# Performance work log

Hardware: AMD Instinct MI355X
Metric: run time of the kernel (lower is better)

Reference implementation:

```python
import jax, jax.numpy as jnp
from jax import lax
import numpy as np

H = 512      # hidden_size
L = 2        # num_layers
IN = 512     # input_size
LAT = 256    # latent_size
B = 256      # batch
S = 256      # seq_length


def setup_inputs() -> dict:
    key = jax.random.key(0)
    ks = jax.random.split(key, 12)
    sd = 0.05
    return {
        "latent": jax.random.normal(ks[0], (B, LAT), dtype=jnp.float32),
        "fc_w": jax.random.normal(ks[1], (H * L * 2, LAT), dtype=jnp.float32) * sd,
        "fc_b": jnp.zeros((H * L * 2,), dtype=jnp.float32),
        "map_w": jax.random.normal(ks[2], (IN, H * 2 * L), dtype=jnp.float32) * sd,
        "map_b": jnp.zeros((IN,), dtype=jnp.float32),
        "wih0": jax.random.normal(ks[3], (4 * H, IN), dtype=jnp.float32) * sd,
        "whh0": jax.random.normal(ks[4], (4 * H, H), dtype=jnp.float32) * sd,
        "bih0": jnp.zeros((4 * H,), dtype=jnp.float32),
        "bhh0": jnp.zeros((4 * H,), dtype=jnp.float32),
        "wih1": jax.random.normal(ks[5], (4 * H, H), dtype=jnp.float32) * sd,
        "whh1": jax.random.normal(ks[6], (4 * H, H), dtype=jnp.float32) * sd,
        "bih1": jnp.zeros((4 * H,), dtype=jnp.float32),
        "bhh1": jnp.zeros((4 * H,), dtype=jnp.float32),
        "seq_length": S,
    }


def _lstm_cell(x, h, c, wih, whh, bih, bhh):
    # torch.nn.LSTMCell gate ordering: i, f, g, o
    g = x @ wih.T + bih + h @ whh.T + bhh
    i, f, gg, o = jnp.split(g, 4, axis=-1)
    c2 = jax.nn.sigmoid(f) * c + jax.nn.sigmoid(i) * jnp.tanh(gg)
    h2 = jax.nn.sigmoid(o) * jnp.tanh(c2)
    return h2, c2


def reference(latent, fc_w, fc_b, map_w, map_b,
              wih0, whh0, bih0, bhh0, wih1, whh1, bih1, bhh1, seq_length):
    bsz = latent.shape[0]
    hid = wih0.shape[0] // 4
    nl = 2
    # dec_hidden = tanh(fc(latent)) -> view(num_layers, B, 2H) -> chunk into (h, c)
    dec = jnp.tanh(latent @ fc_w.T + fc_b)            # (B, 2*L*H)
    dec = dec.reshape(nl, bsz, 2 * hid)               # row-major reinterpret, as torch .view
    h0, c0 = dec[..., :hid], dec[..., hid:]           # each (L, B, H)
    wih = (wih0, wih1); whh = (whh0, whh1)
    bih = (bih0, bih1); bhh = (bhh0, bhh1)

    def step(carry, _):
        h, c = carry
        # cat((h,c), -1).view(B, -1) -- faithful raw reshape across (layer, batch)
        fc_in = jnp.concatenate([h, c], axis=-1).reshape(bsz, -1)  # (B, 2*L*H)
        out = jax.nn.sigmoid(fc_in @ map_w.T + map_b)              # (B, IN)
        x = out
        hs, cs = [], []
        for l in range(nl):
            h2, c2 = _lstm_cell(x, h[l], c[l], wih[l], whh[l], bih[l], bhh[l])
            hs.append(h2); cs.append(c2)
            x = h2
        hn = jnp.tanh(jnp.stack(hs))   # activation_rnn
        cn = jnp.tanh(jnp.stack(cs))   # activation_fc
        return (hn, cn), out

    _, outs = lax.scan(step, (h0, c0), None, length=int(seq_length))
    return outs  # (S, B, IN)
```

## Files before the change

### kernel.cpp

```cpp
#include <hip/hip_runtime.h>

#define SEQ 256

#define WL0     0u
#define WL1     2097152u
#define FCT     4194304u
#define OFF_FC  4718592u
#define OFF_XM  5767168u
#define OFF_X0  5898240u
#define OFF_ARR 6029312u

#define S_AS0 0
#define S_WS0 8704
#define S_AS1 13312
#define S_WS1 22016
#define S_RED 13312
#define S_GS  29952
#define S_TOT 32032

__device__ __forceinline__ float sigf(float x){ return 1.0f/(1.0f + __expf(-x)); }
__device__ __forceinline__ float tanhf_(float x){
  float cx = fminf(fmaxf(x, -15.f), 15.f);
  float e = __expf(2.f*cx);
  return (e-1.f)/(e+1.f);
}

__global__ __launch_bounds__(256) void tr_kernel(const float* __restrict__ src,
                                                 float* __restrict__ dst, int R, int C){
  int i = blockIdx.x*256 + threadIdx.x;
  if (i < R*C){ int r = i / C, c = i - r*C; dst[(size_t)c*R + r] = src[i]; }
}

__global__ __launch_bounds__(256) void wprep(const float* __restrict__ wih0,
                                             const float* __restrict__ whh0,
                                             const float* __restrict__ wih1,
                                             const float* __restrict__ whh1,
                                             float* __restrict__ ws){
  const unsigned idx = blockIdx.x*256u + threadIdx.x;
  const unsigned layer = idx >> 21, rem = idx & 2097151u;
  const unsigned c = rem >> 10, k = rem & 1023u;
  const unsigned j = c >> 2, g = c & 3u;
  const float* wih = layer ? wih1 : wih0;
  const float* whh = layer ? whh1 : whh0;
  const float v = (k < 512u) ? wih[(g*512u + j)*512u + k] : whh[(g*512u + j)*512u + (k - 512u)];
  ws[(layer ? WL1 : WL0) + rem] = v;
}

__global__ __launch_bounds__(256) void init2(const float* __restrict__ latent,
                                             const float* __restrict__ fc_b,
                                             float* __restrict__ ws){
  __shared__ float ls[256];
  const int b = blockIdx.x, tid = threadIdx.x;
  if (tid < 32)
    __hip_atomic_store((unsigned*)(ws + OFF_ARR) + b*32 + tid, 0u,
                       __ATOMIC_RELAXED, __HIP_MEMORY_SCOPE_AGENT);
  ls[tid] = latent[b*256 + tid];
  __syncthreads();
  const float* fT = ws + FCT;
  for (int nc = 0; nc < 8; ++nc){
    const int n = nc*256 + tid;
    float acc = fc_b[n];
    for (int k = 0; k < 256; ++k) acc += ls[k] * fT[k*2048 + n];
    const float v = tanhf_(acc);
    const unsigned f = (unsigned)b*2048u + (unsigned)n;
    const unsigned l = f >> 18, p = (f >> 10) & 255u, q = f & 1023u;
    ws[OFF_FC + (l*128u + (p>>1))*2048u + (p&1u)*1024u + q] = v;
  }
}

__device__ __forceinline__ void gsync(unsigned* arr, unsigned epoch, int tid, int blk){
  __syncthreads();
  if (tid == 0)
    __hip_atomic_store(arr + (unsigned)blk*32u, epoch,
                       __ATOMIC_RELEASE, __HIP_MEMORY_SCOPE_AGENT);
  if (tid < 64){
    unsigned m;
    do {
      const unsigned v0 = __hip_atomic_load(arr + (unsigned)(tid      )*32u, __ATOMIC_RELAXED, __HIP_MEMORY_SCOPE_AGENT);
      const unsigned v1 = __hip_atomic_load(arr + (unsigned)(tid +  64)*32u, __ATOMIC_RELAXED, __HIP_MEMORY_SCOPE_AGENT);
      const unsigned v2 = __hip_atomic_load(arr + (unsigned)(tid + 128)*32u, __ATOMIC_RELAXED, __HIP_MEMORY_SCOPE_AGENT);
      const unsigned v3 = __hip_atomic_load(arr + (unsigned)(tid + 192)*32u, __ATOMIC_RELAXED, __HIP_MEMORY_SCOPE_AGENT);
      const unsigned m01 = v0 < v1 ? v0 : v1;
      const unsigned m23 = v2 < v3 ? v2 : v3;
      m = m01 < m23 ? m01 : m23;
      if (m < epoch) __builtin_amdgcn_s_sleep(2);
    } while (!__all(m >= epoch));
  }
  __syncthreads();
  if (tid == 0) __builtin_amdgcn_fence(__ATOMIC_ACQUIRE, "agent");
  __syncthreads();
}

__device__ __forceinline__ void fma8x8(float acc[8][8], const float4 A0, const float4 A1,
                                       const float4 W0, const float4 W1){
  const float a_[8] = {A0.x,A0.y,A0.z,A0.w,A1.x,A1.y,A1.z,A1.w};
  const float w_[8] = {W0.x,W0.y,W0.z,W0.w,W1.x,W1.y,W1.z,W1.w};
  #pragma unroll
  for (int i=0;i<8;++i)
    #pragma unroll
    for (int j=0;j<8;++j) acc[i][j] = __builtin_fmaf(a_[i], w_[j], acc[i][j]);
}

__device__ __forceinline__ void map_phase(float* sm, const float* __restrict__ FCc,
    const float* __restrict__ map_w, const float* __restrict__ map_b,
    float* __restrict__ XM, float* __restrict__ outp_t, int tid, int r0, int cb)
{
  const int rg = tid & 7;
  const int kg = tid >> 3;
  const int n0 = cb * 8;
  float acc[8][8];
  #pragma unroll
  for (int i=0;i<8;++i){
    #pragma unroll
    for (int j=0;j<8;++j) acc[i][j]=0.f;
  }
  float4 va[8]; float4 vw;

  auto LOADS = [&](int ch){
    #pragma unroll
    for (int it=0; it<8; ++it){
      const int e = tid + it*256, r = e>>5, kq = e&31;
      va[it] = *(const float4*)&FCc[(unsigned)(r0+r)*2048u + (unsigned)(ch*128 + kq*4)];
    }
    { const int n = tid>>5, kq = tid&31;
      vw = *(const float4*)&map_w[(unsigned)(n0+n)*2048u + (unsigned)(ch*128 + kq*4)]; }
  };
  auto STORES = [&](int buf){
    float* A_ = sm + (buf ? S_AS1 : S_AS0);
    float* W_ = sm + (buf ? S_WS1 : S_WS0);
    #pragma unroll
    for (int it=0; it<8; ++it){
      const int e = tid + it*256, r = e>>5, kq = e&31;
      const int col = r ^ ((kq&7)<<2);
      A_[(kq*4+0)*68 + col] = va[it].x;
      A_[(kq*4+1)*68 + col] = va[it].y;
      A_[(kq*4+2)*68 + col] = va[it].z;
      A_[(kq*4+3)*68 + col] = va[it].w;
    }
    { const int n = tid>>5, kq = tid&31;
      const int col = n ^ ((kq&7)<<2);
      W_[(kq*4+0)*36 + col] = vw.x;
      W_[(kq*4+1)*36 + col] = vw.y;
      W_[(kq*4+2)*36 + col] = vw.z;
      W_[(kq*4+3)*36 + col] = vw.w; }
  };
  auto COMPUTE = [&](int buf){
    const float* A_ = sm + (buf ? S_AS1 : S_AS0);
    const float* W_ = sm + (buf ? S_WS1 : S_WS0);
    const int phi = (kg & 7) << 2;
    const int ca0 = (rg*8) ^ phi, ca1 = ca0 ^ 4;
    #pragma unroll
    for (int u=0; u<4; ++u){
      const int k = kg*4 + u;
      const float4 a0 = *(const float4*)&A_[k*68 + ca0];
      const float4 a1 = *(const float4*)&A_[k*68 + ca1];
      const float4 w0 = *(const float4*)&W_[k*36 + phi];
      const float4 w1 = *(const float4*)&W_[k*36 + (phi^4)];
      fma8x8(acc, a0, a1, w0, w1);
    }
  };

  LOADS(0); STORES(1);
  __syncthreads();
  #pragma unroll 1
  for (int ch = 0; ch < 16; ++ch){
    const int buf = (ch & 1) ^ 1;
    if (ch+1 < 16) LOADS(ch+1);
    COMPUTE(buf);
    if (ch+1 < 16) STORES(buf^1);
    __syncthreads();
  }
  float* red = sm + S_RED;
  #pragma unroll
  for (int i=0;i<8;++i){
    #pragma unroll
    for (int j=0;j<8;++j) red[tid*65 + i*8 + j] = acc[i][j];
  }
  __syncthreads();
  #pragma unroll
  for (int s=0;s<2;++s){
    const int o = tid + s*256;
    const int r = o >> 3, nl = o & 7;
    float sum = 0.f;
    #pragma unroll
    for (int kk=0;kk<32;++kk)
      sum += red[((r>>3) + 8*kk)*65 + (r&7)*8 + nl];
    const int n = n0 + nl;
    const float v = sigf(sum + map_b[n]);
    const unsigned off = (unsigned)(r0 + r)*512u + (unsigned)n;
    XM[off] = v;
    outp_t[off] = v;
  }
}

__device__ __forceinline__ void lstm_phase(float* sm, const int l,
    const float* __restrict__ WL, const float* __restrict__ xs,
    const float* __restrict__ FCc, float* __restrict__ FCn,
    float* __restrict__ X0, const float* __restrict__ bih, const float* __restrict__ bhh,
    int tid, int r0, int cb)
{
  const int rg = tid & 7;
  const int ng = (tid >> 3) & 3;
  const int kg = tid >> 5;
  const int c0 = cb * 32;
  float acc[8][8];
  #pragma unroll
  for (int i=0;i<8;++i){
    #pragma unroll
    for (int j=0;j<8;++j) acc[i][j]=0.f;
  }
  float4 va[8], vw4[4];

  auto LOADS = [&](int ch){
    if (ch < 4){
      #pragma unroll
      for (int it=0; it<8; ++it){
        const int e = tid + it*256, r = e>>5, kq = e&31;
        va[it] = *(const float4*)&xs[(unsigned)(r0+r)*512u + (unsigned)(ch*128 + kq*4)];
      }
    } else {
      #pragma unroll
      for (int it=0; it<8; ++it){
        const int e = tid + it*256, r = e>>5, kq = e&31;
        const int b = r0 + r;
        const unsigned q = (unsigned)((ch-4)*128 + kq*4);
        va[it] = *(const float4*)&FCc[(unsigned)((l<<7) + (b>>1))*2048u + (unsigned)(b&1)*1024u + q];
      }
    }
    #pragma unroll
    for (int it=0; it<4; ++it){
      const int e = tid + it*256, n = e>>5, kq = e&31;
      vw4[it] = *(const float4*)&WL[(unsigned)(c0+n)*1024u + (unsigned)(ch*128 + kq*4)];
    }
  };
  auto STORES = [&](int buf){
    float* A_ = sm + (buf ? S_AS1 : S_AS0);
    float* W_ = sm + (buf ? S_WS1 : S_WS0);
    #pragma unroll
    for (int it=0; it<8; ++it){
      const int e = tid + it*256, r = e>>5, kq = e&31;
      const int col = r ^ ((kq&7)<<2);
      A_[(kq*4+0)*68 + col] = va[it].x;
      A_[(kq*4+1)*68 + col] = va[it].y;
      A_[(kq*4+2)*68 + col] = va[it].z;
      A_[(kq*4+3)*68 + col] = va[it].w;
    }
    #pragma unroll
    for (int it=0; it<4; ++it){
      const int e = tid + it*256, n = e>>5, kq = e&31;
      const int col = n ^ ((kq&7)<<2);
      W_[(kq*4+0)*36 + col] = vw4[it].x;
      W_[(kq*4+1)*36 + col] = vw4[it].y;
      W_[(kq*4+2)*36 + col] = vw4[it].z;
      W_[(kq*4+3)*36 + col] = vw4[it].w;
    }
  };
  auto COMPUTE = [&](int buf){
    const float* A_ = sm + (buf ? S_AS1 : S_AS0);
    const float* W_ = sm + (buf ? S_WS1 : S_WS0);
    #pragma unroll
    for (int u=0; u<16; ++u){
      const int k = kg*16 + u;
      const int s = (((kg<<2) + (u>>2)) & 7) << 2;
      const int ca = (rg*8) ^ s;
      const int cw = (ng*8) ^ s;
      const float4 a0 = *(const float4*)&A_[k*68 + ca];
      const float4 a1 = *(const float4*)&A_[k*68 + (ca^4)];
      const float4 w0 = *(const float4*)&W_[k*36 + cw];
      const float4 w1 = *(const float4*)&W_[k*36 + (cw^4)];
      fma8x8(acc, a0, a1, w0, w1);
    }
  };

  LOADS(0); STORES(1);
  __syncthreads();
  #pragma unroll 1
  for (int ch = 0; ch < 8; ++ch){
    const int buf = (ch & 1) ^ 1;
    if (ch+1 < 8) LOADS(ch+1);
    COMPUTE(buf);
    if (ch+1 < 8) STORES(buf^1);
    __syncthreads();
  }

  float* red = sm + S_RED;
  float* gs  = sm + S_GS;
  #pragma unroll
  for (int i=0;i<8;++i){
    #pragma unroll
    for (int j=0;j<8;++j) red[tid*65 + i*8 + j] = acc[i][j];
  }
  __syncthreads();
  #pragma unroll
  for (int s=0;s<8;++s){
    const int o = tid + s*256;
    const int r = o >> 5, c = o & 31;
    float sum = 0.f;
    #pragma unroll
    for (int kk=0;kk<8;++kk)
      sum += red[((r>>3) + 8*(c>>3) + 32*kk)*65 + (r&7)*8 + (c&7)];
    gs[c*65 + r] = sum;
  }
  __syncthreads();
  const int r = tid & 63, j0 = tid >> 6;
  const int row = r0 + r;
  const unsigned srow = (unsigned)((l<<7) + (row>>1))*2048u + (unsigned)(row&1)*1024u;
  #pragma unroll
  for (int jj=0;jj<2;++jj){
    const int jl = j0 + jj*4;
    const int jg = cb*8 + jl;
    const float gi = gs[(jl*4+0)*65 + r] + bih[jg]       + bhh[jg];
    const float gf = gs[(jl*4+1)*65 + r] + bih[512+jg]   + bhh[512+jg];
    const float gg = gs[(jl*4+2)*65 + r] + bih[1024+jg]  + bhh[1024+jg];
    const float go = gs[(jl*4+3)*65 + r] + bih[1536+jg]  + bhh[1536+jg];
    const float cp = FCc[srow + 512u + (unsigned)jg];
    const float c2 = sigf(gf)*cp + sigf(gi)*tanhf_(gg);
    const float h2 = sigf(go)*tanhf_(c2);
    if (l == 0) X0[(unsigned)row*512u + (unsigned)jg] = h2;
    FCn[srow + (unsigned)jg]        = tanhf_(h2);
    FCn[srow + 512u + (unsigned)jg] = tanhf_(c2);
  }
}

__launch_bounds__(256, 1)
__global__ void persist(const float* __restrict__ map_w, const float* __restrict__ map_b,
                        const float* __restrict__ bih0, const float* __restrict__ bhh0,
                        const float* __restrict__ bih1, const float* __restrict__ bhh1,
                        float* __restrict__ ws, float* __restrict__ outp)
{
  __shared__ float sm[S_TOT];
  const int tid = threadIdx.x;
  const int blk = blockIdx.x;
  const int cb = ((blk & 7) << 3) | ((blk >> 3) & 7);
  const int rb = blk >> 6;
  const int r0 = rb * 64;
  float* FC = ws + OFF_FC;
  float* XM = ws + OFF_XM;
  float* X0 = ws + OFF_X0;
  unsigned* arr = (unsigned*)(ws + OFF_ARR);
  unsigned nsync = 0;

  #pragma unroll 1
  for (int t = 0; t < SEQ; ++t){
    const unsigned cur = (unsigned)(t & 1);
    const float* FCc = FC + cur*524288u;
    float* FCn = FC + (cur^1u)*524288u;

    map_phase(sm, FCc, map_w, map_b, XM, outp + (size_t)t*131072u, tid, r0, cb);
    if (t == SEQ-1) break;
    gsync(arr, ++nsync, tid, blk);
    lstm_phase(sm, 0, ws + WL0, XM, FCc, FCn, X0, bih0, bhh0, tid, r0, cb);
    gsync(arr, ++nsync, tid, blk);
    lstm_phase(sm, 1, ws + WL1, X0, FCc, FCn, X0, bih1, bhh1, tid, r0, cb);
    gsync(arr, ++nsync, tid, blk);
  }
}

extern "C" void kernel_launch(void* const* d_in, const int* in_sizes, int n_in,
                              void* d_out, int out_size, void* d_ws, size_t ws_size,
                              hipStream_t stream)
{
  (void)in_sizes; (void)n_in; (void)out_size; (void)ws_size;
  const float* latent = (const float*)d_in[0];
  const float* fc_w   = (const float*)d_in[1];
  const float* fc_b   = (const float*)d_in[2];
  const float* map_w  = (const float*)d_in[3];
  const float* map_b  = (const float*)d_in[4];
  const float* wih0   = (const float*)d_in[5];
  const float* whh0   = (const float*)d_in[6];
  const float* bih0   = (const float*)d_in[7];
  const float* bhh0   = (const float*)d_in[8];
  const float* wih1   = (const float*)d_in[9];
  const float* whh1   = (const float*)d_in[10];
  const float* bih1   = (const float*)d_in[11];
  const float* bhh1   = (const float*)d_in[12];
  float* ws = (float*)d_ws;
  float* outp = (float*)d_out;

  tr_kernel<<<2048,256,0,stream>>>(fc_w, ws + FCT, 2048, 256);
  wprep<<<16384,256,0,stream>>>(wih0, whh0, wih1, whh1, ws);
  init2<<<256,256,0,stream>>>(latent, fc_b, ws);

  void* args[8];
  args[0] = (void*)&map_w; args[1] = (void*)&map_b;
  args[2] = (void*)&bih0;  args[3] = (void*)&bhh0;
  args[4] = (void*)&bih1;  args[5] = (void*)&bhh1;
  args[6] = (void*)&ws;    args[7] = (void*)&outp;
  hipError_t e = hipLaunchCooperativeKernel((const void*)persist, dim3(256), dim3(256),
                                            args, 0, stream);
  if (e != hipSuccess){
    persist<<<dim3(256), dim3(256), 0, stream>>>(map_w, map_b, bih0, bhh0,
                                                 bih1, bhh1, ws, outp);
  }
}
```

Baseline: 38.95 ms.

## Double threads per persistent block and halve per-thread register tile

Each persistent block now runs 512 threads instead of 256, and each thread computes an 8x4 accumulator tile instead of 8x8, with the load, store and reduction index maps rewritten to match. The aim is more latency hiding per CU during the latency-bound recurrent GEMMs, plus shorter per-thread serial FMA chains. The trade-off is a wider K-split reduction through shared memory (more partials), larger LDS scratch and more threads taking part in each barrier. The grid-wide sync code must still work with the larger block, since only the first 64 threads poll.

```diff
diff --git a/kernel.cpp b/kernel.cpp
--- a/kernel.cpp
+++ b/kernel.cpp
@@ -15,8 +15,8 @@
 #define S_AS1 13312
 #define S_WS1 22016
 #define S_RED 13312
-#define S_GS  29952
-#define S_TOT 32032
+#define S_GS  30208
+#define S_TOT 32288
 
 __device__ __forceinline__ float sigf(float x){ return 1.0f/(1.0f + __expf(-x)); }
 __device__ __forceinline__ float tanhf_(float x){
@@ -91,14 +91,14 @@
   __syncthreads();
 }
 
-__device__ __forceinline__ void fma8x8(float acc[8][8], const float4 A0, const float4 A1,
-                                       const float4 W0, const float4 W1){
+__device__ __forceinline__ void fma8x4(float acc[8][4], const float4 A0, const float4 A1,
+                                       const float4 W0){
   const float a_[8] = {A0.x,A0.y,A0.z,A0.w,A1.x,A1.y,A1.z,A1.w};
-  const float w_[8] = {W0.x,W0.y,W0.z,W0.w,W1.x,W1.y,W1.z,W1.w};
+  const float w_[4] = {W0.x,W0.y,W0.z,W0.w};
   #pragma unroll
   for (int i=0;i<8;++i)
     #pragma unroll
-    for (int j=0;j<8;++j) acc[i][j] = __builtin_fmaf(a_[i], w_[j], acc[i][j]);
+    for (int j=0;j<4;++j) acc[i][j] = __builtin_fmaf(a_[i], w_[j], acc[i][j]);
 }
 
 __device__ __forceinline__ void map_phase(float* sm, const float* __restrict__ FCc,
@@ -106,38 +106,39 @@
     float* __restrict__ XM, float* __restrict__ outp_t, int tid, int r0, int cb)
 {
   const int rg = tid & 7;
-  const int kg = tid >> 3;
+  const int ng = (tid >> 3) & 1;
+  const int kg = tid >> 4;
   const int n0 = cb * 8;
-  float acc[8][8];
+  float acc[8][4];
   #pragma unroll
   for (int i=0;i<8;++i){
     #pragma unroll
-    for (int j=0;j<8;++j) acc[i][j]=0.f;
-  }
-  float4 va[8]; float4 vw;
+    for (int j=0;j<4;++j) acc[i][j]=0.f;
+  }
+  float4 va[4]; float4 vw;
 
   auto LOADS = [&](int ch){
     #pragma unroll
-    for (int it=0; it<8; ++it){
-      const int e = tid + it*256, r = e>>5, kq = e&31;
+    for (int it=0; it<4; ++it){
+      const int e = tid + it*512, r = e>>5, kq = e&31;
       va[it] = *(const float4*)&FCc[(unsigned)(r0+r)*2048u + (unsigned)(ch*128 + kq*4)];
     }
-    { const int n = tid>>5, kq = tid&31;
+    if (tid < 256){ const int n = tid>>5, kq = tid&31;
       vw = *(const float4*)&map_w[(unsigned)(n0+n)*2048u + (unsigned)(ch*128 + kq*4)]; }
   };
   auto STORES = [&](int buf){
     float* A_ = sm + (buf ? S_AS1 : S_AS0);
     float* W_ = sm + (buf ? S_WS1 : S_WS0);
     #pragma unroll
-    for (int it=0; it<8; ++it){
-      const int e = tid + it*256, r = e>>5, kq = e&31;
+    for (int it=0; it<4; ++it){
+      const int e = tid + it*512, r = e>>5, kq = e&31;
       const int col = r ^ ((kq&7)<<2);
       A_[(kq*4+0)*68 + col] = va[it].x;
       A_[(kq*4+1)*68 + col] = va[it].y;
       A_[(kq*4+2)*68 + col] = va[it].z;
       A_[(kq*4+3)*68 + col] = va[it].w;
     }
-    { const int n = tid>>5, kq = tid&31;
+    if (tid < 256){ const int n = tid>>5, kq = tid&31;
       const int col = n ^ ((kq&7)<<2);
       W_[(kq*4+0)*36 + col] = vw.x;
       W_[(kq*4+1)*36 + col] = vw.y;
@@ -149,14 +150,14 @@
     const float* W_ = sm + (buf ? S_WS1 : S_WS0);
     const int phi = (kg & 7) << 2;
     const int ca0 = (rg*8) ^ phi, ca1 = ca0 ^ 4;
+    const int cw = (ng*4) ^ phi;
     #pragma unroll
     for (int u=0; u<4; ++u){
       const int k = kg*4 + u;
       const float4 a0 = *(const float4*)&A_[k*68 + ca0];
       const float4 a1 = *(const float4*)&A_[k*68 + ca1];
-      const float4 w0 = *(const float4*)&W_[k*36 + phi];
-      const float4 w1 = *(const float4*)&W_[k*36 + (phi^4)];
-      fma8x8(acc, a0, a1, w0, w1);
+      const float4 w0 = *(const float4*)&W_[k*36 + cw];
+      fma8x4(acc, a0, a1, w0);
     }
   };
 
@@ -174,17 +175,16 @@
   #pragma unroll
   for (int i=0;i<8;++i){
     #pragma unroll
-    for (int j=0;j<8;++j) red[tid*65 + i*8 + j] = acc[i][j];
-  }
-  __syncthreads();
-  #pragma unroll
-  for (int s=0;s<2;++s){
-    const int o = tid + s*256;
+    for (int j=0;j<4;++j) red[tid*33 + i*4 + j] = acc[i][j];
+  }
+  __syncthreads();
+  {
+    const int o = tid;
     const int r = o >> 3, nl = o & 7;
     float sum = 0.f;
     #pragma unroll
     for (int kk=0;kk<32;++kk)
-      sum += red[((r>>3) + 8*kk)*65 + (r&7)*8 + nl];
+      sum += red[((r>>3) + 8*(nl>>2) + 16*kk)*33 + (r&7)*4 + (nl&3)];
     const int n = n0 + nl;
     const float v = sigf(sum + map_b[n]);
     const unsigned off = (unsigned)(r0 + r)*512u + (unsigned)n;
@@ -200,36 +200,36 @@
     int tid, int r0, int cb)
 {
   const int rg = tid & 7;
-  const int ng = (tid >> 3) & 3;
-  const int kg = tid >> 5;
+  const int ng = (tid >> 3) & 7;
+  const int kg = tid >> 6;
   const int c0 = cb * 32;
-  float acc[8][8];
+  float acc[8][4];
   #pragma unroll
   for (int i=0;i<8;++i){
     #pragma unroll
-    for (int j=0;j<8;++j) acc[i][j]=0.f;
-  }
-  float4 va[8], vw4[4];
+    for (int j=0;j<4;++j) acc[i][j]=0.f;
+  }
+  float4 va[4], vw4[2];
 
   auto LOADS = [&](int ch){
     if (ch < 4){
       #pragma unroll
-      for (int it=0; it<8; ++it){
-        const int e = tid + it*256, r = e>>5, kq = e&31;
+      for (int it=0; it<4; ++it){
+        const int e = tid + it*512, r = e>>5, kq = e&31;
         va[it] = *(const float4*)&xs[(unsigned)(r0+r)*512u + (unsigned)(ch*128 + kq*4)];
       }
     } else {
       #pragma unroll
-      for (int it=0; it<8; ++it){
-        const int e = tid + it*256, r = e>>5, kq = e&31;
+      for (int it=0; it<4; ++it){
+        const int e = tid + it*512, r = e>>5, kq = e&31;
         const int b = r0 + r;
         const unsigned q = (unsigned)((ch-4)*128 + kq*4);
         va[it] = *(const float4*)&FCc[(unsigned)((l<<7) + (b>>1))*2048u + (unsigned)(b&1)*1024u + q];
       }
     }
     #pragma unroll
-    for (int it=0; it<4; ++it){
-      const int e = tid + it*256, n = e>>5, kq = e&31;
+    for (int it=0; it<2; ++it){
+      const int e = tid + it*512, n = e>>5, kq = e&31;
       vw4[it] = *(const float4*)&WL[(unsigned)(c0+n)*1024u + (unsigned)(ch*128 + kq*4)];
     }
   };
@@ -237,8 +237,8 @@
     float* A_ = sm + (buf ? S_AS1 : S_AS0);
     float* W_ = sm + (buf ? S_WS1 : S_WS0);
     #pragma unroll
-    for (int it=0; it<8; ++it){
-      const int e = tid + it*256, r = e>>5, kq = e&31;
+    for (int it=0; it<4; ++it){
+      const int e = tid + it*512, r = e>>5, kq = e&31;
       const int col = r ^ ((kq&7)<<2);
       A_[(kq*4+0)*68 + col] = va[it].x;
       A_[(kq*4+1)*68 + col] = va[it].y;
@@ -246,8 +246,8 @@
       A_[(kq*4+3)*68 + col] = va[it].w;
     }
     #pragma unroll
-    for (int it=0; it<4; ++it){
-      const int e = tid + it*256, n = e>>5, kq = e&31;
+    for (int it=0; it<2; ++it){
+      const int e = tid + it*512, n = e>>5, kq = e&31;
       const int col = n ^ ((kq&7)<<2);
       W_[(kq*4+0)*36 + col] = vw4[it].x;
       W_[(kq*4+1)*36 + col] = vw4[it].y;
@@ -263,12 +263,11 @@
       const int k = kg*16 + u;
       const int s = (((kg<<2) + (u>>2)) & 7) << 2;
       const int ca = (rg*8) ^ s;
-      const int cw = (ng*8) ^ s;
+      const int cw = (ng*4) ^ s;
       const float4 a0 = *(const float4*)&A_[k*68 + ca];
       const float4 a1 = *(const float4*)&A_[k*68 + (ca^4)];
       const float4 w0 = *(const float4*)&W_[k*36 + cw];
-      const float4 w1 = *(const float4*)&W_[k*36 + (cw^4)];
-      fma8x8(acc, a0, a1, w0, w1);
+      fma8x4(acc, a0, a1, w0);
     }
   };
 
@@ -288,41 +287,37 @@
   #pragma unroll
   for (int i=0;i<8;++i){
     #pragma unroll
-    for (int j=0;j<8;++j) red[tid*65 + i*8 + j] = acc[i][j];
-  }
-  __syncthreads();
-  #pragma unroll
-  for (int s=0;s<8;++s){
-    const int o = tid + s*256;
+    for (int j=0;j<4;++j) red[tid*33 + i*4 + j] = acc[i][j];
+  }
+  __syncthreads();
+  #pragma unroll
+  for (int s=0;s<4;++s){
+    const int o = tid + s*512;
     const int r = o >> 5, c = o & 31;
     float sum = 0.f;
     #pragma unroll
     for (int kk=0;kk<8;++kk)
-      sum += red[((r>>3) + 8*(c>>3) + 32*kk)*65 + (r&7)*8 + (c&7)];
+      sum += red[((r>>3) + 8*(c>>2) + 64*kk)*33 + (r&7)*4 + (c&3)];
     gs[c*65 + r] = sum;
   }
   __syncthreads();
   const int r = tid & 63, j0 = tid >> 6;
   const int row = r0 + r;
   const unsigned srow = (unsigned)((l<<7) + (row>>1))*2048u + (unsigned)(row&1)*1024u;
-  #pragma unroll
-  for (int jj=0;jj<2;++jj){
-    const int jl = j0 + jj*4;
-    const int jg = cb*8 + jl;
-    const float gi = gs[(jl*4+0)*65 + r] + bih[jg]       + bhh[jg];
-    const float gf = gs[(jl*4+1)*65 + r] + bih[512+jg]   + bhh[512+jg];
-    const float gg = gs[(jl*4+2)*65 + r] + bih[1024+jg]  + bhh[1024+jg];
-    const float go = gs[(jl*4+3)*65 + r] + bih[1536+jg]  + bhh[1536+jg];
-    const float cp = FCc[srow + 512u + (unsigned)jg];
-    const float c2 = sigf(gf)*cp + sigf(gi)*tanhf_(gg);
-    const float h2 = sigf(go)*tanhf_(c2);
-    if (l == 0) X0[(unsigned)row*512u + (unsigned)jg] = h2;
-    FCn[srow + (unsigned)jg]        = tanhf_(h2);
-    FCn[srow + 512u + (unsigned)jg] = tanhf_(c2);
-  }
-}
-
-__launch_bounds__(256, 1)
+  const int jg = cb*8 + j0;
+  const float gi = gs[(j0*4+0)*65 + r] + bih[jg]       + bhh[jg];
+  const float gf = gs[(j0*4+1)*65 + r] + bih[512+jg]   + bhh[512+jg];
+  const float gg = gs[(j0*4+2)*65 + r] + bih[1024+jg]  + bhh[1024+jg];
+  const float go = gs[(j0*4+3)*65 + r] + bih[1536+jg]  + bhh[1536+jg];
+  const float cp = FCc[srow + 512u + (unsigned)jg];
+  const float c2 = sigf(gf)*cp + sigf(gi)*tanhf_(gg);
+  const float h2 = sigf(go)*tanhf_(c2);
+  if (l == 0) X0[(unsigned)row*512u + (unsigned)jg] = h2;
+  FCn[srow + (unsigned)jg]        = tanhf_(h2);
+  FCn[srow + 512u + (unsigned)jg] = tanhf_(c2);
+}
+
+__launch_bounds__(512, 2)
 __global__ void persist(const float* __restrict__ map_w, const float* __restrict__ map_b,
                         const float* __restrict__ bih0, const float* __restrict__ bhh0,
                         const float* __restrict__ bih1, const float* __restrict__ bhh1,
@@ -386,10 +381,10 @@
   args[2] = (void*)&bih0;  args[3] = (void*)&bhh0;
   args[4] = (void*)&bih1;  args[5] = (void*)&bhh1;
   args[6] = (void*)&ws;    args[7] = (void*)&outp;
-  hipError_t e = hipLaunchCooperativeKernel((const void*)persist, dim3(256), dim3(256),
+  hipError_t e = hipLaunchCooperativeKernel((const void*)persist, dim3(256), dim3(512),
                                             args, 0, stream);
   if (e != hipSuccess){
-    persist<<<dim3(256), dim3(256), 0, stream>>>(map_w, map_b, bih0, bhh0,
+    persist<<<dim3(256), dim3(512), 0, stream>>>(map_w, map_b, bih0, bhh0,
                                                  bih1, bhh1, ws, outp);
   }
 }
```

New measurement: 52.51 ms. 1.35x slower.
